# Performance work log

Measured on AMD Instinct MI355X. Metric: run time of the kernel, lower is better.

## Reference

```python
import jax, jax.numpy as jnp
import numpy as np
from jax import lax

B, C_IN, H = 64, 3, 64
K_FEAT, KSIZE, STRIDE = 24, 8, 8
G_IN, G_HID, F_HID, OUT = 52, 256, 256, 1


def setup_inputs() -> dict:
    key = jax.random.key(0)
    ks = jax.random.split(key, 8)
    s = lambda fan_in: 1.0 / np.sqrt(fan_in)
    return {
        "image": jax.random.normal(ks[0], (B, C_IN, H, H), jnp.float32),
        "conv_w": jax.random.normal(ks[1], (K_FEAT, C_IN, KSIZE, KSIZE), jnp.float32) * s(C_IN * KSIZE * KSIZE),
        "conv_b": jnp.zeros((K_FEAT,), jnp.float32),
        "g_w1": jax.random.normal(ks[2], (G_IN, G_HID), jnp.float32) * s(G_IN),
        "g_b1": jnp.zeros((G_HID,), jnp.float32),
        "g_w2": jax.random.normal(ks[3], (G_HID, G_HID), jnp.float32) * s(G_HID),
        "g_b2": jnp.zeros((G_HID,), jnp.float32),
        "f_w1": jax.random.normal(ks[4], (G_HID, F_HID), jnp.float32) * s(G_HID),
        "f_b1": jnp.zeros((F_HID,), jnp.float32),
        "f_w2": jax.random.normal(ks[5], (F_HID, OUT), jnp.float32) * s(F_HID),
        "f_b2": jnp.zeros((OUT,), jnp.float32),
    }


def reference(image, conv_w, conv_b, g_w1, g_b1, g_w2, g_b2, f_w1, f_b1, f_w2, f_b2):
    # feature_extractor: conv k8/s8 + ReLU -> (B, k, d, d)
    x = lax.conv_general_dilated(image, conv_w, (STRIDE, STRIDE), "VALID",
                                 dimension_numbers=("NCHW", "OIHW", "NCHW"))
    x = jax.nn.relu(x + conv_b[None, :, None, None])
    b, k, d, _ = x.shape
    # coordinate channels: x varies along columns, y along rows (linspace(-1,1,d))
    coord = jnp.linspace(-1.0, 1.0, d, dtype=x.dtype)
    cx = jnp.broadcast_to(coord[None, None, None, :], (b, 1, d, d))
    cy = jnp.broadcast_to(coord[None, None, :, None], (b, 1, d, d))
    x = jnp.concatenate([x, cx, cy], axis=1)          # (B, k+2, d, d)
    k2 = k + 2
    x = x.reshape(b, k2, d * d).transpose(0, 2, 1)     # (B, d^2, k+2)
    # all-pairs: pair (i, j) -> concat(x[:, j], x[:, i])  (matches repeat/cat in torch)
    left = jnp.broadcast_to(x[:, None, :, :], (b, d * d, d * d, k2))
    right = jnp.broadcast_to(x[:, :, None, :], (b, d * d, d * d, k2))
    pairs = jnp.concatenate([left, right], axis=-1)    # (B, d^2, d^2, 2(k+2))
    # g: shared MLP over pairs
    h = jax.nn.relu(pairs @ g_w1 + g_b1)
    h = jax.nn.relu(h @ g_w2 + g_b2)                   # (B, d^2, d^2, 256)
    pooled = jnp.sum(h, axis=(1, 2))                   # sum over d^4 pairs -> (B, 256)
    # f: head MLP
    h = jax.nn.relu(pooled @ f_w1 + f_b1)
    return h @ f_w2 + f_b2                             # (B, 1)
```

## Files before the change

### kernel.cpp

```cpp
#include <hip/hip_runtime.h>
#include <hip/hip_bf16.h>
#include <stdint.h>


typedef float f32x4 __attribute__((ext_vector_type(4)));
typedef float f32x2 __attribute__((ext_vector_type(2)));
typedef short short8 __attribute__((ext_vector_type(8)));
typedef int   int4v  __attribute__((ext_vector_type(4)));

#define NB 4

__device__ __forceinline__ uint32_t cvt_pk_bf16(float lo, float hi) {
    uint32_t r;
    asm("v_cvt_pk_bf16_f32 %0, %1, %2" : "=v"(r) : "v"(lo), "v"(hi));
    return r;
}
__device__ __forceinline__ f32x2 relu2(f32x2 a) {
    f32x2 z = (f32x2){0.f, 0.f};
    return __builtin_elementwise_max(a, z);
}
__device__ __forceinline__ void spin_eq(int* p, int val) {
    while (__hip_atomic_load(p, __ATOMIC_ACQUIRE, __HIP_MEMORY_SCOPE_WORKGROUP) != val)
        __builtin_amdgcn_s_sleep(1);
    __builtin_amdgcn_sched_barrier(0);
}
__device__ __forceinline__ void flag_release_add(int* p, int lane) {
    asm volatile("s_waitcnt lgkmcnt(0)" ::: "memory");
    if (lane == 0)
        __hip_atomic_fetch_add(p, 1, __ATOMIC_RELEASE, __HIP_MEMORY_SCOPE_WORKGROUP);
}

__global__ void k12_front(const float* __restrict__ img, const float* __restrict__ cw,
                          const float* __restrict__ cb, const float* __restrict__ w1,
                          const float* __restrict__ b1, const float* __restrict__ w2,
                          float* __restrict__ u, float* __restrict__ v,
                          short* __restrict__ w2f) {
    int g = blockIdx.x;
    int t = threadIdx.x;
    if (g >= 256) {
        int fi = (g - 256) * 4 + (t >> 6);
        int l = t & 63;
        int ks = fi >> 4, ni2 = fi & 15;
        int n  = ni2 * 16 + (l & 15);
        int k0 = ks * 32 + (l >> 4) * 8;
        float f[8];
        #pragma unroll
        for (int e = 0; e < 8; ++e) f[e] = w2[(k0 + e) * 256 + n];
        union { short8 s; uint32_t w[4]; } A;
        A.w[0] = cvt_pk_bf16(f[0], f[1]);
        A.w[1] = cvt_pk_bf16(f[2], f[3]);
        A.w[2] = cvt_pk_bf16(f[4], f[5]);
        A.w[3] = cvt_pk_bf16(f[6], f[7]);
        *(short8*)(w2f + (fi * 64 + l) * 8) = A.s;
        return;
    }
    __shared__ float xs[16][26];
    int b = g >> 2, q = g & 3, p0 = q * 16;

    for (int idx = t; idx < 416; idx += 256) {
        int pl = idx / 26;
        int ch = idx - pl * 26;
        int pos = p0 + pl;
        int r = pos >> 3, c = pos & 7;
        float val;
        if (ch < 24) {
            float s = cb[ch];
            #pragma unroll
            for (int ci = 0; ci < 3; ++ci)
                #pragma unroll
                for (int kr = 0; kr < 8; ++kr) {
                    const float* ip = img + ((b * 3 + ci) * 64 + r * 8 + kr) * 64 + c * 8;
                    const float* wp = cw + ((ch * 3 + ci) * 8 + kr) * 8;
                    #pragma unroll
                    for (int kc = 0; kc < 8; ++kc) s += ip[kc] * wp[kc];
                }
            val = fmaxf(s, 0.f);
        } else if (ch == 24) {
            val = -1.f + (2.f / 7.f) * (float)c;
        } else {
            val = -1.f + (2.f / 7.f) * (float)r;
        }
        xs[pl][ch] = val;
    }
    __syncthreads();

    int c = t;
    float bc = b1[c];
    float su[16], sv[16];
    #pragma unroll
    for (int r = 0; r < 16; ++r) { su[r] = bc; sv[r] = 0.f; }
    #pragma unroll 2
    for (int k = 0; k < 26; ++k) {
        float wu = w1[k * 256 + c];
        float wv2 = w1[(26 + k) * 256 + c];
        #pragma unroll
        for (int r = 0; r < 16; ++r) {
            float xv = xs[r][k];
            su[r] += xv * wu;
            sv[r] += xv * wv2;
        }
    }
    #pragma unroll
    for (int r = 0; r < 16; ++r) {
        int bj = b * 64 + p0 + r;
        u[bj * 256 + c] = su[r];
        v[bj * 256 + c] = sv[r];
    }
}

#define C_READ(A, KS)                                                  \
    { const char* hx = ((KS) & 1) ? hO : hE;                           \
      A[0] = *(const short8*)(hx + ((KS) >> 1) * 128);                 \
      A[1] = *(const short8*)(hx + 8192  + ((KS) >> 1) * 128);         \
      A[2] = *(const short8*)(hx + 16384 + ((KS) >> 1) * 128);         \
      A[3] = *(const short8*)(hx + 24576 + ((KS) >> 1) * 128); }

#define C_MFMA(A, KS)                                                  \
    { acc[0][0] = __builtin_amdgcn_mfma_f32_16x16x32_bf16(A[0], Bf[KS][0], acc[0][0], 0,0,0); \
      acc[1][0] = __builtin_amdgcn_mfma_f32_16x16x32_bf16(A[1], Bf[KS][0], acc[1][0], 0,0,0); \
      acc[2][0] = __builtin_amdgcn_mfma_f32_16x16x32_bf16(A[2], Bf[KS][0], acc[2][0], 0,0,0); \
      acc[3][0] = __builtin_amdgcn_mfma_f32_16x16x32_bf16(A[3], Bf[KS][0], acc[3][0], 0,0,0); \
      acc[0][1] = __builtin_amdgcn_mfma_f32_16x16x32_bf16(A[0], Bf[KS][1], acc[0][1], 0,0,0); \
      acc[1][1] = __builtin_amdgcn_mfma_f32_16x16x32_bf16(A[1], Bf[KS][1], acc[1][1], 0,0,0); \
      acc[2][1] = __builtin_amdgcn_mfma_f32_16x16x32_bf16(A[2], Bf[KS][1], acc[2][1], 0,0,0); \
      acc[3][1] = __builtin_amdgcn_mfma_f32_16x16x32_bf16(A[3], Bf[KS][1], acc[3][1], 0,0,0); \
      acc[0][2] = __builtin_amdgcn_mfma_f32_16x16x32_bf16(A[0], Bf[KS][2], acc[0][2], 0,0,0); \
      acc[1][2] = __builtin_amdgcn_mfma_f32_16x16x32_bf16(A[1], Bf[KS][2], acc[1][2], 0,0,0); \
      acc[2][2] = __builtin_amdgcn_mfma_f32_16x16x32_bf16(A[2], Bf[KS][2], acc[2][2], 0,0,0); \
      acc[3][2] = __builtin_amdgcn_mfma_f32_16x16x32_bf16(A[3], Bf[KS][2], acc[3][2], 0,0,0); \
      acc[0][3] = __builtin_amdgcn_mfma_f32_16x16x32_bf16(A[0], Bf[KS][3], acc[0][3], 0,0,0); \
      acc[1][3] = __builtin_amdgcn_mfma_f32_16x16x32_bf16(A[1], Bf[KS][3], acc[1][3], 0,0,0); \
      acc[2][3] = __builtin_amdgcn_mfma_f32_16x16x32_bf16(A[2], Bf[KS][3], acc[2][3], 0,0,0); \
      acc[3][3] = __builtin_amdgcn_mfma_f32_16x16x32_bf16(A[3], Bf[KS][3], acc[3][3], 0,0,0); }

__global__ __launch_bounds__(512, 2) void k3_pairs(
        const float* __restrict__ u, const float* __restrict__ v,
        const short* __restrict__ w2f, const float* __restrict__ b2,
        float* __restrict__ part) {
    __shared__ short h1s[NB][64 * 256];
    __shared__ float vs[16][2][128];
    __shared__ int prod_cnt[16];
    __shared__ int cons_cnt[16];
    int t = threadIdx.x;
    int lane = t & 63, wv = t >> 6;
    int blk = blockIdx.x;
    int b = blk & 63, i0 = (blk >> 6) * 16;

    if (t < 16) { prod_cnt[t] = 0; cons_cnt[t] = 0; }

    {
        int q = t >> 5, c8 = (t & 31) * 8;
        const float* vr = v + (b * 64 + i0 + q) * 256 + c8;
        *(float4*)&vs[q][0][(t & 31) * 4] = *(const float4*)vr;
        *(float4*)&vs[q][1][(t & 31) * 4] = *(const float4*)(vr + 4);
    }
    __syncthreads();

    if (wv < 4) {
        int col8 = t & 31, rq = t >> 5;
        const float* up = u + (b * 64 + rq * 8) * 256 + col8 * 8;
        f32x4 u0[8], u1[8];
        #pragma unroll
        for (int rr = 0; rr < 8; ++rr) {
            u0[rr] = *(const f32x4*)(up + rr * 256);
            u1[rr] = *(const f32x4*)(up + rr * 256 + 4);
        }
        int wbase = rq * 8 * 512;
        int c16 = col8 * 16;

        #pragma unroll 1
        for (int q = 0; q < 16; ++q) {
            if (q >= NB) spin_eq(&cons_cnt[q - NB], 4);
            char* wbuf = (char*)h1s[q & (NB - 1)] + wbase;
            f32x4 va = *(const f32x4*)&vs[q][0][col8 * 4];
            f32x4 vb = *(const f32x4*)&vs[q][1][col8 * 4];
            #pragma unroll
            for (int rr = 0; rr < 8; ++rr) {
                f32x2 a0 = relu2((f32x2){u0[rr].x, u0[rr].y} + (f32x2){va.x, va.y});
                f32x2 a1 = relu2((f32x2){u0[rr].z, u0[rr].w} + (f32x2){va.z, va.w});
                f32x2 a2 = relu2((f32x2){u1[rr].x, u1[rr].y} + (f32x2){vb.x, vb.y});
                f32x2 a3 = relu2((f32x2){u1[rr].z, u1[rr].w} + (f32x2){vb.z, vb.w});
                int4v d;
                d.x = (int)cvt_pk_bf16(a0.x, a0.y);
                d.y = (int)cvt_pk_bf16(a1.x, a1.y);
                d.z = (int)cvt_pk_bf16(a2.x, a2.y);
                d.w = (int)cvt_pk_bf16(a3.x, a3.y);
                *(int4v*)(wbuf + rr * 512 + (c16 ^ (rr << 4))) = d;
            }
            flag_release_add(&prod_cnt[q], lane);
        }
    } else {
        int wc = wv - 4;
        int lr = lane & 15, lg = lane >> 4;

        short8 Bf[8][4];
        #pragma unroll
        for (int ks = 0; ks < 8; ++ks)
            #pragma unroll
            for (int cg = 0; cg < 4; ++cg)
                Bf[ks][cg] = *(const short8*)(w2f + ((ks * 16 + wc * 4 + cg) * 64 + lane) * 8);

        f32x2 bias2[4];
        #pragma unroll
        for (int cg = 0; cg < 4; ++cg) {
            float bv = b2[wc * 64 + cg * 16 + lr];
            bias2[cg] = (f32x2){bv, bv};
        }

        int XB = (lg * 16) ^ ((lr & 7) << 4);
        int rE0 = lr * 512 + XB;
        int rO0 = lr * 512 + (XB ^ 64);

        f32x2 csum2[4];
        #pragma unroll
        for (int cg = 0; cg < 4; ++cg) csum2[cg] = (f32x2){0.f, 0.f};

        __builtin_amdgcn_s_setprio(1);
        #pragma unroll 1
        for (int q = 0; q < 16; ++q) {
            spin_eq(&prod_cnt[q], 4);
            const char* base = (const char*)h1s[q & (NB - 1)];
            const char* hE = base + rE0;
            const char* hO = base + rO0;

            f32x4 acc[4][4];
            #pragma unroll
            for (int mi = 0; mi < 4; ++mi)
                #pragma unroll
                for (int cg = 0; cg < 4; ++cg) acc[mi][cg] = (f32x4){0.f, 0.f, 0.f, 0.f};

            short8 Aa[4], Ab[4];
            C_READ(Aa, 0) C_READ(Ab, 1)
            C_MFMA(Aa, 0) C_READ(Aa, 2)
            C_MFMA(Ab, 1) C_READ(Ab, 3)
            C_MFMA(Aa, 2) C_READ(Aa, 4)
            C_MFMA(Ab, 3) C_READ(Ab, 5)
            C_MFMA(Aa, 4) C_READ(Aa, 6)
            C_MFMA(Ab, 5) C_READ(Ab, 7)
            C_MFMA(Aa, 6)
            C_MFMA(Ab, 7)

            #pragma unroll
            for (int cg = 0; cg < 4; ++cg) {
                #pragma unroll
                for (int mi = 0; mi < 4; ++mi) {
                    f32x2 lo = relu2((f32x2){acc[mi][cg].x, acc[mi][cg].y} + bias2[cg]);
                    f32x2 hi = relu2((f32x2){acc[mi][cg].z, acc[mi][cg].w} + bias2[cg]);
                    csum2[cg] = csum2[cg] + lo + hi;
                }
            }
            flag_release_add(&cons_cnt[q], lane);
        }
        __builtin_amdgcn_s_setprio(0);

        #pragma unroll
        for (int cg = 0; cg < 4; ++cg) {
            float s = csum2[cg].x + csum2[cg].y;
            s += __shfl_xor(s, 16);
            s += __shfl_xor(s, 32);
            if (lane < 16) part[(blk * 4 + wc) * 64 + cg * 16 + lr] = s;
        }
    }
}

__global__ void k5_head(const float* __restrict__ part, const float* __restrict__ fw1,
                        const float* __restrict__ fb1, const float* __restrict__ fw2,
                        const float* __restrict__ fb2, float* __restrict__ out) {
    __shared__ float P[256];
    __shared__ float wsum[4];
    int b = blockIdx.x, t = threadIdx.x;
    int wc = t >> 6, cl = t & 63;
    float s0 = 0.f;
    #pragma unroll
    for (int g = 0; g < 4; ++g)
        s0 += part[((b + 64 * g) * 4 + wc) * 64 + cl];
    P[t] = s0;
    __syncthreads();
    float a0 = 0.f, a1 = 0.f, a2 = 0.f, a3 = 0.f;
    for (int k = 0; k < 64; ++k) {
        a0 += P[k]       * fw1[k * 256 + t];
        a1 += P[k + 64]  * fw1[(k + 64) * 256 + t];
        a2 += P[k + 128] * fw1[(k + 128) * 256 + t];
        a3 += P[k + 192] * fw1[(k + 192) * 256 + t];
    }
    float h = fmaxf(fb1[t] + a0 + a1 + a2 + a3, 0.f);
    float p = h * fw2[t];
    #pragma unroll
    for (int off = 32; off >= 1; off >>= 1) p += __shfl_xor(p, off);
    if ((t & 63) == 0) wsum[t >> 6] = p;
    __syncthreads();
    if (t == 0) out[b] = wsum[0] + wsum[1] + wsum[2] + wsum[3] + fb2[0];
}

extern "C" void kernel_launch(void* const* d_in, const int* in_sizes, int n_in,
                              void* d_out, int out_size, void* d_ws, size_t ws_size,
                              hipStream_t stream) {
    const float* image  = (const float*)d_in[0];
    const float* conv_w = (const float*)d_in[1];
    const float* conv_b = (const float*)d_in[2];
    const float* g_w1   = (const float*)d_in[3];
    const float* g_b1   = (const float*)d_in[4];
    const float* g_w2   = (const float*)d_in[5];
    const float* g_b2   = (const float*)d_in[6];
    const float* f_w1   = (const float*)d_in[7];
    const float* f_b1   = (const float*)d_in[8];
    const float* f_w2   = (const float*)d_in[9];
    const float* f_b2   = (const float*)d_in[10];
    float* out = (float*)d_out;

    char* ws = (char*)d_ws;
    float* u    = (float*)(ws + 0);
    float* v    = (float*)(ws + 4194304);
    short* w2f  = (short*)(ws + 8388608);
    float* part = (float*)(ws + 8519680);

    k12_front<<<288, 256, 0, stream>>>(image, conv_w, conv_b, g_w1, g_b1, g_w2,
                                       u, v, w2f);
    k3_pairs<<<256, 512, 0, stream>>>(u, v, w2f, g_b2, part);
    k5_head<<<64, 256, 0, stream>>>(part, f_w1, f_b1, f_w2, f_b2, out);
}
```

Measured before the change: 60.30 us.

## Fuse conv and first-layer projection into the pairs kernel, recomputing per block

Removes the separate front kernel. Each pairs block now computes the conv features, the u/v projections into shared memory (reusing the h1 buffer space), and converts w2 to bf16 fragments inline. This drops one launch and the global round trip for u, v and w2f. In exchange, the conv and u projection are recomputed 4 times per batch (once per i0 block), and setprio is narrowed to the MFMA section only.

```diff
diff --git a/kernel.cpp b/kernel.cpp
--- a/kernel.cpp
+++ b/kernel.cpp
@@ -28,84 +28,6 @@
     asm volatile("s_waitcnt lgkmcnt(0)" ::: "memory");
     if (lane == 0)
         __hip_atomic_fetch_add(p, 1, __ATOMIC_RELEASE, __HIP_MEMORY_SCOPE_WORKGROUP);
-}
-
-__global__ void k12_front(const float* __restrict__ img, const float* __restrict__ cw,
-                          const float* __restrict__ cb, const float* __restrict__ w1,
-                          const float* __restrict__ b1, const float* __restrict__ w2,
-                          float* __restrict__ u, float* __restrict__ v,
-                          short* __restrict__ w2f) {
-    int g = blockIdx.x;
-    int t = threadIdx.x;
-    if (g >= 256) {
-        int fi = (g - 256) * 4 + (t >> 6);
-        int l = t & 63;
-        int ks = fi >> 4, ni2 = fi & 15;
-        int n  = ni2 * 16 + (l & 15);
-        int k0 = ks * 32 + (l >> 4) * 8;
-        float f[8];
-        #pragma unroll
-        for (int e = 0; e < 8; ++e) f[e] = w2[(k0 + e) * 256 + n];
-        union { short8 s; uint32_t w[4]; } A;
-        A.w[0] = cvt_pk_bf16(f[0], f[1]);
-        A.w[1] = cvt_pk_bf16(f[2], f[3]);
-        A.w[2] = cvt_pk_bf16(f[4], f[5]);
-        A.w[3] = cvt_pk_bf16(f[6], f[7]);
-        *(short8*)(w2f + (fi * 64 + l) * 8) = A.s;
-        return;
-    }
-    __shared__ float xs[16][26];
-    int b = g >> 2, q = g & 3, p0 = q * 16;
-
-    for (int idx = t; idx < 416; idx += 256) {
-        int pl = idx / 26;
-        int ch = idx - pl * 26;
-        int pos = p0 + pl;
-        int r = pos >> 3, c = pos & 7;
-        float val;
-        if (ch < 24) {
-            float s = cb[ch];
-            #pragma unroll
-            for (int ci = 0; ci < 3; ++ci)
-                #pragma unroll
-                for (int kr = 0; kr < 8; ++kr) {
-                    const float* ip = img + ((b * 3 + ci) * 64 + r * 8 + kr) * 64 + c * 8;
-                    const float* wp = cw + ((ch * 3 + ci) * 8 + kr) * 8;
-                    #pragma unroll
-                    for (int kc = 0; kc < 8; ++kc) s += ip[kc] * wp[kc];
-                }
-            val = fmaxf(s, 0.f);
-        } else if (ch == 24) {
-            val = -1.f + (2.f / 7.f) * (float)c;
-        } else {
-            val = -1.f + (2.f / 7.f) * (float)r;
-        }
-        xs[pl][ch] = val;
-    }
-    __syncthreads();
-
-    int c = t;
-    float bc = b1[c];
-    float su[16], sv[16];
-    #pragma unroll
-    for (int r = 0; r < 16; ++r) { su[r] = bc; sv[r] = 0.f; }
-    #pragma unroll 2
-    for (int k = 0; k < 26; ++k) {
-        float wu = w1[k * 256 + c];
-        float wv2 = w1[(26 + k) * 256 + c];
-        #pragma unroll
-        for (int r = 0; r < 16; ++r) {
-            float xv = xs[r][k];
-            su[r] += xv * wu;
-            sv[r] += xv * wv2;
-        }
-    }
-    #pragma unroll
-    for (int r = 0; r < 16; ++r) {
-        int bj = b * 64 + p0 + r;
-        u[bj * 256 + c] = su[r];
-        v[bj * 256 + c] = sv[r];
-    }
 }
 
 #define C_READ(A, KS)                                                  \
@@ -133,12 +55,13 @@
       acc[2][3] = __builtin_amdgcn_mfma_f32_16x16x32_bf16(A[2], Bf[KS][3], acc[2][3], 0,0,0); \
       acc[3][3] = __builtin_amdgcn_mfma_f32_16x16x32_bf16(A[3], Bf[KS][3], acc[3][3], 0,0,0); }
 
-__global__ __launch_bounds__(512, 2) void k3_pairs(
-        const float* __restrict__ u, const float* __restrict__ v,
-        const short* __restrict__ w2f, const float* __restrict__ b2,
-        float* __restrict__ part) {
+__global__ __launch_bounds__(512, 2) void k_main(
+        const float* __restrict__ img, const float* __restrict__ cw,
+        const float* __restrict__ cb, const float* __restrict__ w1,
+        const float* __restrict__ b1, const float* __restrict__ w2,
+        const float* __restrict__ b2, float* __restrict__ part) {
     __shared__ short h1s[NB][64 * 256];
-    __shared__ float vs[16][2][128];
+    __shared__ float vsm[16][256];
     __shared__ int prod_cnt[16];
     __shared__ int cons_cnt[16];
     int t = threadIdx.x;
@@ -148,32 +71,83 @@
 
     if (t < 16) { prod_cnt[t] = 0; cons_cnt[t] = 0; }
 
-    {
-        int q = t >> 5, c8 = (t & 31) * 8;
-        const float* vr = v + (b * 64 + i0 + q) * 256 + c8;
-        *(float4*)&vs[q][0][(t & 31) * 4] = *(const float4*)vr;
-        *(float4*)&vs[q][1][(t & 31) * 4] = *(const float4*)(vr + 4);
+    float* xs = (float*)&h1s[0][0];
+    float* us = (float*)((char*)&h1s[0][0] + 32768);
+
+    for (int idx = t; idx < 1664; idx += 512) {
+        int pos = idx / 26;
+        int ch  = idx - pos * 26;
+        int r = pos >> 3, c = pos & 7;
+        float val;
+        if (ch < 24) {
+            float s = cb[ch];
+            #pragma unroll
+            for (int ci = 0; ci < 3; ++ci)
+                #pragma unroll
+                for (int kr = 0; kr < 8; ++kr) {
+                    const float* ip = img + ((b * 3 + ci) * 64 + r * 8 + kr) * 64 + c * 8;
+                    const float* wp = cw + ((ch * 3 + ci) * 8 + kr) * 8;
+                    float4 a0 = *(const float4*)ip;
+                    float4 a1 = *(const float4*)(ip + 4);
+                    float4 q0 = *(const float4*)wp;
+                    float4 q1 = *(const float4*)(wp + 4);
+                    s += a0.x * q0.x + a0.y * q0.y + a0.z * q0.z + a0.w * q0.w
+                       + a1.x * q1.x + a1.y * q1.y + a1.z * q1.z + a1.w * q1.w;
+                }
+            val = fmaxf(s, 0.f);
+        } else if (ch == 24) {
+            val = -1.f + (2.f / 7.f) * (float)c;
+        } else {
+            val = -1.f + (2.f / 7.f) * (float)r;
+        }
+        xs[pos * 26 + ch] = val;
     }
     __syncthreads();
 
+    {
+        int c = t & 255, half = t >> 8;
+        float su[32], sv[8];
+        float bc = b1[c];
+        #pragma unroll
+        for (int r = 0; r < 32; ++r) su[r] = bc;
+        #pragma unroll
+        for (int r = 0; r < 8; ++r) sv[r] = 0.f;
+        int ur0 = half * 32;
+        int vr0 = i0 + half * 8;
+        #pragma unroll 2
+        for (int k = 0; k < 26; ++k) {
+            float wu  = w1[k * 256 + c];
+            float wvv = w1[(26 + k) * 256 + c];
+            #pragma unroll
+            for (int r = 0; r < 32; ++r) su[r] += xs[(ur0 + r) * 26 + k] * wu;
+            #pragma unroll
+            for (int r = 0; r < 8; ++r)  sv[r] += xs[(vr0 + r) * 26 + k] * wvv;
+        }
+        #pragma unroll
+        for (int r = 0; r < 32; ++r) us[(ur0 + r) * 256 + c] = su[r];
+        #pragma unroll
+        for (int r = 0; r < 8; ++r)  vsm[half * 8 + r][c] = sv[r];
+    }
+    __syncthreads();
+
     if (wv < 4) {
         int col8 = t & 31, rq = t >> 5;
-        const float* up = u + (b * 64 + rq * 8) * 256 + col8 * 8;
         f32x4 u0[8], u1[8];
         #pragma unroll
         for (int rr = 0; rr < 8; ++rr) {
-            u0[rr] = *(const f32x4*)(up + rr * 256);
-            u1[rr] = *(const f32x4*)(up + rr * 256 + 4);
+            u0[rr] = *(const f32x4*)(us + (rq * 8 + rr) * 256 + col8 * 8);
+            u1[rr] = *(const f32x4*)(us + (rq * 8 + rr) * 256 + col8 * 8 + 4);
         }
         int wbase = rq * 8 * 512;
         int c16 = col8 * 16;
+        __syncthreads();
 
         #pragma unroll 1
         for (int q = 0; q < 16; ++q) {
             if (q >= NB) spin_eq(&cons_cnt[q - NB], 4);
             char* wbuf = (char*)h1s[q & (NB - 1)] + wbase;
-            f32x4 va = *(const f32x4*)&vs[q][0][col8 * 4];
-            f32x4 vb = *(const f32x4*)&vs[q][1][col8 * 4];
+            f32x4 va = *(const f32x4*)&vsm[q][col8 * 8];
+            f32x4 vb = *(const f32x4*)&vsm[q][col8 * 8 + 4];
             #pragma unroll
             for (int rr = 0; rr < 8; ++rr) {
                 f32x2 a0 = relu2((f32x2){u0[rr].x, u0[rr].y} + (f32x2){va.x, va.y});
@@ -197,8 +171,17 @@
         #pragma unroll
         for (int ks = 0; ks < 8; ++ks)
             #pragma unroll
-            for (int cg = 0; cg < 4; ++cg)
-                Bf[ks][cg] = *(const short8*)(w2f + ((ks * 16 + wc * 4 + cg) * 64 + lane) * 8);
+            for (int cg = 0; cg < 4; ++cg) {
+                int n  = wc * 64 + cg * 16 + lr;
+                int k0 = ks * 32 + lg * 8;
+                const float* wp = w2 + k0 * 256 + n;
+                union { short8 s; uint32_t w[4]; } A;
+                A.w[0] = cvt_pk_bf16(wp[0],        wp[256]);
+                A.w[1] = cvt_pk_bf16(wp[2 * 256],  wp[3 * 256]);
+                A.w[2] = cvt_pk_bf16(wp[4 * 256],  wp[5 * 256]);
+                A.w[3] = cvt_pk_bf16(wp[6 * 256],  wp[7 * 256]);
+                Bf[ks][cg] = A.s;
+            }
 
         f32x2 bias2[4];
         #pragma unroll
@@ -215,7 +198,8 @@
         #pragma unroll
         for (int cg = 0; cg < 4; ++cg) csum2[cg] = (f32x2){0.f, 0.f};
 
-        __builtin_amdgcn_s_setprio(1);
+        __syncthreads();
+
         #pragma unroll 1
         for (int q = 0; q < 16; ++q) {
             spin_eq(&prod_cnt[q], 4);
@@ -231,6 +215,7 @@
 
             short8 Aa[4], Ab[4];
             C_READ(Aa, 0) C_READ(Ab, 1)
+            __builtin_amdgcn_s_setprio(1);
             C_MFMA(Aa, 0) C_READ(Aa, 2)
             C_MFMA(Ab, 1) C_READ(Ab, 3)
             C_MFMA(Aa, 2) C_READ(Aa, 4)
@@ -239,6 +224,7 @@
             C_MFMA(Ab, 5) C_READ(Ab, 7)
             C_MFMA(Aa, 6)
             C_MFMA(Ab, 7)
+            __builtin_amdgcn_s_setprio(0);
 
             #pragma unroll
             for (int cg = 0; cg < 4; ++cg) {
@@ -251,7 +237,6 @@
             }
             flag_release_add(&cons_cnt[q], lane);
         }
-        __builtin_amdgcn_s_setprio(0);
 
         #pragma unroll
         for (int cg = 0; cg < 4; ++cg) {
@@ -308,14 +293,9 @@
     const float* f_b2   = (const float*)d_in[10];
     float* out = (float*)d_out;
 
-    char* ws = (char*)d_ws;
-    float* u    = (float*)(ws + 0);
-    float* v    = (float*)(ws + 4194304);
-    short* w2f  = (short*)(ws + 8388608);
-    float* part = (float*)(ws + 8519680);
-
-    k12_front<<<288, 256, 0, stream>>>(image, conv_w, conv_b, g_w1, g_b1, g_w2,
-                                       u, v, w2f);
-    k3_pairs<<<256, 512, 0, stream>>>(u, v, w2f, g_b2, part);
+    float* part = (float*)d_ws;
+
+    k_main<<<256, 512, 0, stream>>>(image, conv_w, conv_b, g_w1, g_b1, g_w2,
+                                    g_b2, part);
     k5_head<<<64, 256, 0, stream>>>(part, f_w1, f_b1, f_w2, f_b2, out);
 }
```

Result: slower. 92.60 us (+53.6%).

## Widen pair kernel to 8 consumer waves with MFMA-fragment-ordered h1 layout

Applied to the files above, without the earlier changes.

The pairs kernel grows from 512 to 768 threads. Eight consumer waves each compute 32 output columns instead of four waves covering 64, which halves the accumulator and B-fragment registers per wave. Producers now hold u pre-packed as bf16 and write h1 tiles directly in MFMA A-fragment order, so consumers read linearly without XOR swizzles. The setprio scope is narrowed to the MFMA section and the partial-sum layout plus head indexing are updated. The risk is that u is now rounded to bf16 before the add, which adds precision error, and doubling the consumer count makes each producer stage sync with twice as many waves.

```diff
diff --git a/kernel.cpp b/kernel.cpp
--- a/kernel.cpp
+++ b/kernel.cpp
@@ -18,6 +18,13 @@
 __device__ __forceinline__ f32x2 relu2(f32x2 a) {
     f32x2 z = (f32x2){0.f, 0.f};
     return __builtin_elementwise_max(a, z);
+}
+__device__ __forceinline__ uint32_t fuse2(uint32_t up, float vlo, float vhi) {
+    f32x2 uu;
+    uu.x = __uint_as_float(up << 16);
+    uu.y = __uint_as_float(up & 0xFFFF0000u);
+    f32x2 r = relu2(uu + (f32x2){vlo, vhi});
+    return cvt_pk_bf16(r.x, r.y);
 }
 __device__ __forceinline__ void spin_eq(int* p, int val) {
     while (__hip_atomic_load(p, __ATOMIC_ACQUIRE, __HIP_MEMORY_SCOPE_WORKGROUP) != val)
@@ -109,11 +116,10 @@
 }
 
 #define C_READ(A, KS)                                                  \
-    { const char* hx = ((KS) & 1) ? hO : hE;                           \
-      A[0] = *(const short8*)(hx + ((KS) >> 1) * 128);                 \
-      A[1] = *(const short8*)(hx + 8192  + ((KS) >> 1) * 128);         \
-      A[2] = *(const short8*)(hx + 16384 + ((KS) >> 1) * 128);         \
-      A[3] = *(const short8*)(hx + 24576 + ((KS) >> 1) * 128); }
+    { A[0] = *(const short8*)(cb0 + (KS) * 1024);                      \
+      A[1] = *(const short8*)(cb0 + 8192  + (KS) * 1024);              \
+      A[2] = *(const short8*)(cb0 + 16384 + (KS) * 1024);              \
+      A[3] = *(const short8*)(cb0 + 24576 + (KS) * 1024); }
 
 #define C_MFMA(A, KS)                                                  \
     { acc[0][0] = __builtin_amdgcn_mfma_f32_16x16x32_bf16(A[0], Bf[KS][0], acc[0][0], 0,0,0); \
@@ -123,114 +129,98 @@
       acc[0][1] = __builtin_amdgcn_mfma_f32_16x16x32_bf16(A[0], Bf[KS][1], acc[0][1], 0,0,0); \
       acc[1][1] = __builtin_amdgcn_mfma_f32_16x16x32_bf16(A[1], Bf[KS][1], acc[1][1], 0,0,0); \
       acc[2][1] = __builtin_amdgcn_mfma_f32_16x16x32_bf16(A[2], Bf[KS][1], acc[2][1], 0,0,0); \
-      acc[3][1] = __builtin_amdgcn_mfma_f32_16x16x32_bf16(A[3], Bf[KS][1], acc[3][1], 0,0,0); \
-      acc[0][2] = __builtin_amdgcn_mfma_f32_16x16x32_bf16(A[0], Bf[KS][2], acc[0][2], 0,0,0); \
-      acc[1][2] = __builtin_amdgcn_mfma_f32_16x16x32_bf16(A[1], Bf[KS][2], acc[1][2], 0,0,0); \
-      acc[2][2] = __builtin_amdgcn_mfma_f32_16x16x32_bf16(A[2], Bf[KS][2], acc[2][2], 0,0,0); \
-      acc[3][2] = __builtin_amdgcn_mfma_f32_16x16x32_bf16(A[3], Bf[KS][2], acc[3][2], 0,0,0); \
-      acc[0][3] = __builtin_amdgcn_mfma_f32_16x16x32_bf16(A[0], Bf[KS][3], acc[0][3], 0,0,0); \
-      acc[1][3] = __builtin_amdgcn_mfma_f32_16x16x32_bf16(A[1], Bf[KS][3], acc[1][3], 0,0,0); \
-      acc[2][3] = __builtin_amdgcn_mfma_f32_16x16x32_bf16(A[2], Bf[KS][3], acc[2][3], 0,0,0); \
-      acc[3][3] = __builtin_amdgcn_mfma_f32_16x16x32_bf16(A[3], Bf[KS][3], acc[3][3], 0,0,0); }
-
-__global__ __launch_bounds__(512, 2) void k3_pairs(
+      acc[3][1] = __builtin_amdgcn_mfma_f32_16x16x32_bf16(A[3], Bf[KS][1], acc[3][1], 0,0,0); }
+
+__global__ __launch_bounds__(768, 3) void k3_pairs(
         const float* __restrict__ u, const float* __restrict__ v,
         const short* __restrict__ w2f, const float* __restrict__ b2,
         float* __restrict__ part) {
     __shared__ short h1s[NB][64 * 256];
-    __shared__ float vs[16][2][128];
+    __shared__ float vs[16][256];
     __shared__ int prod_cnt[16];
     __shared__ int cons_cnt[16];
     int t = threadIdx.x;
     int lane = t & 63, wv = t >> 6;
+    int lr = lane & 15, lg = lane >> 4;
     int blk = blockIdx.x;
     int b = blk & 63, i0 = (blk >> 6) * 16;
 
     if (t < 16) { prod_cnt[t] = 0; cons_cnt[t] = 0; }
 
-    {
+    if (t < 512) {
         int q = t >> 5, c8 = (t & 31) * 8;
         const float* vr = v + (b * 64 + i0 + q) * 256 + c8;
-        *(float4*)&vs[q][0][(t & 31) * 4] = *(const float4*)vr;
-        *(float4*)&vs[q][1][(t & 31) * 4] = *(const float4*)(vr + 4);
-    }
-    __syncthreads();
+        *(float4*)&vs[q][c8]     = *(const float4*)vr;
+        *(float4*)&vs[q][c8 + 4] = *(const float4*)(vr + 4);
+    }
 
     if (wv < 4) {
-        int col8 = t & 31, rq = t >> 5;
-        const float* up = u + (b * 64 + rq * 8) * 256 + col8 * 8;
-        f32x4 u0[8], u1[8];
-        #pragma unroll
-        for (int rr = 0; rr < 8; ++rr) {
-            u0[rr] = *(const f32x4*)(up + rr * 256);
-            u1[rr] = *(const f32x4*)(up + rr * 256 + 4);
-        }
-        int wbase = rq * 8 * 512;
-        int c16 = col8 * 16;
+        uint32_t upk[8][4];
+        #pragma unroll
+        for (int j = 0; j < 8; ++j) {
+            int fid = j * 4 + wv;
+            int row = (fid >> 3) * 16 + lr;
+            int k0 = (fid & 7) * 32 + lg * 8;
+            const float* up = u + (b * 64 + row) * 256 + k0;
+            f32x4 x0 = *(const f32x4*)up;
+            f32x4 x1 = *(const f32x4*)(up + 4);
+            upk[j][0] = cvt_pk_bf16(x0.x, x0.y);
+            upk[j][1] = cvt_pk_bf16(x0.z, x0.w);
+            upk[j][2] = cvt_pk_bf16(x1.x, x1.y);
+            upk[j][3] = cvt_pk_bf16(x1.z, x1.w);
+        }
+        __syncthreads();
 
         #pragma unroll 1
         for (int q = 0; q < 16; ++q) {
-            if (q >= NB) spin_eq(&cons_cnt[q - NB], 4);
-            char* wbuf = (char*)h1s[q & (NB - 1)] + wbase;
-            f32x4 va = *(const f32x4*)&vs[q][0][col8 * 4];
-            f32x4 vb = *(const f32x4*)&vs[q][1][col8 * 4];
-            #pragma unroll
-            for (int rr = 0; rr < 8; ++rr) {
-                f32x2 a0 = relu2((f32x2){u0[rr].x, u0[rr].y} + (f32x2){va.x, va.y});
-                f32x2 a1 = relu2((f32x2){u0[rr].z, u0[rr].w} + (f32x2){va.z, va.w});
-                f32x2 a2 = relu2((f32x2){u1[rr].x, u1[rr].y} + (f32x2){vb.x, vb.y});
-                f32x2 a3 = relu2((f32x2){u1[rr].z, u1[rr].w} + (f32x2){vb.z, vb.w});
+            if (q >= NB) spin_eq(&cons_cnt[q - NB], 8);
+            char* base = (char*)h1s[q & (NB - 1)] + lane * 16;
+            #pragma unroll
+            for (int j = 0; j < 8; ++j) {
+                int fid = j * 4 + wv;
+                int k0 = (fid & 7) * 32 + lg * 8;
+                f32x4 v0 = *(const f32x4*)&vs[q][k0];
+                f32x4 v1 = *(const f32x4*)&vs[q][k0 + 4];
                 int4v d;
-                d.x = (int)cvt_pk_bf16(a0.x, a0.y);
-                d.y = (int)cvt_pk_bf16(a1.x, a1.y);
-                d.z = (int)cvt_pk_bf16(a2.x, a2.y);
-                d.w = (int)cvt_pk_bf16(a3.x, a3.y);
-                *(int4v*)(wbuf + rr * 512 + (c16 ^ (rr << 4))) = d;
+                d.x = (int)fuse2(upk[j][0], v0.x, v0.y);
+                d.y = (int)fuse2(upk[j][1], v0.z, v0.w);
+                d.z = (int)fuse2(upk[j][2], v1.x, v1.y);
+                d.w = (int)fuse2(upk[j][3], v1.z, v1.w);
+                *(int4v*)(base + fid * 1024) = d;
             }
             flag_release_add(&prod_cnt[q], lane);
         }
     } else {
         int wc = wv - 4;
-        int lr = lane & 15, lg = lane >> 4;
-
-        short8 Bf[8][4];
+
+        short8 Bf[8][2];
         #pragma unroll
         for (int ks = 0; ks < 8; ++ks)
             #pragma unroll
-            for (int cg = 0; cg < 4; ++cg)
-                Bf[ks][cg] = *(const short8*)(w2f + ((ks * 16 + wc * 4 + cg) * 64 + lane) * 8);
-
-        f32x2 bias2[4];
-        #pragma unroll
-        for (int cg = 0; cg < 4; ++cg) {
-            float bv = b2[wc * 64 + cg * 16 + lr];
-            bias2[cg] = (f32x2){bv, bv};
-        }
-
-        int XB = (lg * 16) ^ ((lr & 7) << 4);
-        int rE0 = lr * 512 + XB;
-        int rO0 = lr * 512 + (XB ^ 64);
-
-        f32x2 csum2[4];
-        #pragma unroll
-        for (int cg = 0; cg < 4; ++cg) csum2[cg] = (f32x2){0.f, 0.f};
-
-        __builtin_amdgcn_s_setprio(1);
+            for (int cg = 0; cg < 2; ++cg)
+                Bf[ks][cg] = *(const short8*)(w2f + ((ks * 16 + wc * 2 + cg) * 64 + lane) * 8);
+
+        float bias[2];
+        #pragma unroll
+        for (int cg = 0; cg < 2; ++cg) bias[cg] = b2[wc * 32 + cg * 16 + lr];
+
+        float csum[2] = {0.f, 0.f};
+        __syncthreads();
+
         #pragma unroll 1
         for (int q = 0; q < 16; ++q) {
             spin_eq(&prod_cnt[q], 4);
-            const char* base = (const char*)h1s[q & (NB - 1)];
-            const char* hE = base + rE0;
-            const char* hO = base + rO0;
-
-            f32x4 acc[4][4];
+            const char* cb0 = (const char*)h1s[q & (NB - 1)] + lane * 16;
+
+            f32x4 acc[4][2];
             #pragma unroll
             for (int mi = 0; mi < 4; ++mi)
                 #pragma unroll
-                for (int cg = 0; cg < 4; ++cg) acc[mi][cg] = (f32x4){0.f, 0.f, 0.f, 0.f};
+                for (int cg = 0; cg < 2; ++cg) acc[mi][cg] = (f32x4){0.f, 0.f, 0.f, 0.f};
 
             short8 Aa[4], Ab[4];
             C_READ(Aa, 0) C_READ(Ab, 1)
+            __builtin_amdgcn_s_setprio(1);
             C_MFMA(Aa, 0) C_READ(Aa, 2)
             C_MFMA(Ab, 1) C_READ(Ab, 3)
             C_MFMA(Aa, 2) C_READ(Aa, 4)
@@ -239,26 +229,27 @@
             C_MFMA(Ab, 5) C_READ(Ab, 7)
             C_MFMA(Aa, 6)
             C_MFMA(Ab, 7)
-
-            #pragma unroll
-            for (int cg = 0; cg < 4; ++cg) {
+            __builtin_amdgcn_s_setprio(0);
+
+            #pragma unroll
+            for (int cg = 0; cg < 2; ++cg) {
+                float s = 0.f;
                 #pragma unroll
-                for (int mi = 0; mi < 4; ++mi) {
-                    f32x2 lo = relu2((f32x2){acc[mi][cg].x, acc[mi][cg].y} + bias2[cg]);
-                    f32x2 hi = relu2((f32x2){acc[mi][cg].z, acc[mi][cg].w} + bias2[cg]);
-                    csum2[cg] = csum2[cg] + lo + hi;
-                }
+                for (int mi = 0; mi < 4; ++mi)
+                    #pragma unroll
+                    for (int r = 0; r < 4; ++r)
+                        s += fmaxf(acc[mi][cg][r] + bias[cg], 0.f);
+                csum[cg] += s;
             }
             flag_release_add(&cons_cnt[q], lane);
         }
-        __builtin_amdgcn_s_setprio(0);
-
-        #pragma unroll
-        for (int cg = 0; cg < 4; ++cg) {
-            float s = csum2[cg].x + csum2[cg].y;
+
+        #pragma unroll
+        for (int cg = 0; cg < 2; ++cg) {
+            float s = csum[cg];
             s += __shfl_xor(s, 16);
             s += __shfl_xor(s, 32);
-            if (lane < 16) part[(blk * 4 + wc) * 64 + cg * 16 + lr] = s;
+            if (lane < 16) part[(blk * 8 + wc) * 32 + cg * 16 + lr] = s;
         }
     }
 }
@@ -269,11 +260,11 @@
     __shared__ float P[256];
     __shared__ float wsum[4];
     int b = blockIdx.x, t = threadIdx.x;
-    int wc = t >> 6, cl = t & 63;
+    int wc = t >> 5, cl = t & 31;
     float s0 = 0.f;
     #pragma unroll
     for (int g = 0; g < 4; ++g)
-        s0 += part[((b + 64 * g) * 4 + wc) * 64 + cl];
+        s0 += part[((b + 64 * g) * 8 + wc) * 32 + cl];
     P[t] = s0;
     __syncthreads();
     float a0 = 0.f, a1 = 0.f, a2 = 0.f, a3 = 0.f;
@@ -316,6 +307,6 @@
 
     k12_front<<<288, 256, 0, stream>>>(image, conv_w, conv_b, g_w1, g_b1, g_w2,
                                        u, v, w2f);
-    k3_pairs<<<256, 512, 0, stream>>>(u, v, w2f, g_b2, part);
+    k3_pairs<<<256, 768, 0, stream>>>(u, v, w2f, g_b2, part);
     k5_head<<<64, 256, 0, stream>>>(part, f_w1, f_b1, f_w2, f_b2, out);
 }
```

Result: no change. 60.25 us (-0.1%).
